# Performance work log

Measured on AMD Instinct MI355X. Metric: run time of the kernel, lower is better.

## Reference

```python
import jax, jax.numpy as jnp
import numpy as np

B, S, DIM = 2, 2048, 2048
H, DH = 16, 128            # head_dim = dim // n_heads; decop_rot_dim == head_dim (required by the view)
LKV, LQ = 512, 1024        # latent kv / q compression dims


def setup_inputs() -> dict:
    key = jax.random.key(0)
    ks = jax.random.split(key, 12)
    w = lambda k, shape: jax.random.normal(k, shape, jnp.float32) * 0.02
    x = jax.random.normal(ks[0], (B, S, DIM), jnp.float32)
    # rotary table: angles[t, i] = t * 10000^(-2i/DH), complex passed as cos/sin pair
    inv_freq = 1.0 / (10000.0 ** (np.arange(0, DH, 2, dtype=np.float64) / DH))
    ang = np.outer(np.arange(S, dtype=np.float64), inv_freq)  # [S, DH/2]
    return {
        "x": x,
        "freq_cos": jnp.asarray(np.cos(ang), jnp.float32),
        "freq_sin": jnp.asarray(np.sin(ang), jnp.float32),
        "w_lq": w(ks[1], (LQ, DIM)),
        "w_lkv": w(ks[2], (LKV, DIM)),
        "w_q": w(ks[3], (H * DH, LQ)),
        "w_k": w(ks[4], (H * DH, LKV)),
        "w_v": w(ks[5], (H * DH, LKV)),
        "w_qr": w(ks[6], (H * DH, LQ)),
        "b_qr": w(ks[7], (H * DH,)),
        "w_kr": w(ks[8], (H * DH, DIM)),
        "b_kr": w(ks[9], (H * DH,)),
        "w_o": w(ks[10], (DIM, H * DH)),
        "b_o": w(ks[11], (DIM,)),
    }


def _rope(t, freq):
    # t: [B,S,H,DH]; freq: [S,DH/2] complex. Pairs (even,odd) along last dim rotated.
    b, s, h, d = t.shape
    tc = t.astype(jnp.float32).reshape(b, s, h, d // 2, 2)
    tc = jax.lax.complex(tc[..., 0], tc[..., 1]) * freq[None, :, None, :]
    return jnp.stack([jnp.real(tc), jnp.imag(tc)], axis=-1).reshape(b, s, h, d).astype(t.dtype)


def reference(x, freq_cos, freq_sin, w_lq, w_lkv, w_q, w_k, w_v, w_qr, b_qr, w_kr, b_kr, w_o, b_o):
    b, s, _ = x.shape
    freq = jax.lax.complex(freq_cos, freq_sin)          # [S, DH/2]
    cq = x @ w_lq.T                                      # [B,S,LQ]
    ckv = x @ w_lkv.T                                    # [B,S,LKV]
    q = (cq @ w_q.T).reshape(b, s, H, DH)
    qr = _rope((cq @ w_qr.T + b_qr).reshape(b, s, H, DH), freq)
    k = (ckv @ w_k.T).reshape(b, s, H, DH)
    kr = _rope((x @ w_kr.T + b_kr).reshape(b, s, H, DH), freq)
    v = (ckv @ w_v.T).reshape(b, s, H, DH)
    q = jnp.concatenate([q, qr], axis=-1)                # [B,S,H,2*DH]
    k = jnp.concatenate([k, kr], axis=-1)
    # note: scale uses sqrt(head_dim), NOT sqrt(2*head_dim), faithful to source
    scores = jnp.einsum('bqhd,bkhd->bhqk', q, k) / jnp.sqrt(jnp.float32(DH))
    att = jax.nn.softmax(scores.astype(jnp.float32), axis=-1).astype(q.dtype)
    out = jnp.einsum('bhqk,bkhd->bqhd', att, v).reshape(b, s, H * DH)
    return out @ w_o.T + b_o
```

## Files before the change

### kernel.cpp

```cpp
#include <hip/hip_runtime.h>
#include <hip/hip_bf16.h>


#define Bb 2
#define Ss 2048
#define DIMd 2048
#define Hh 16
#define DHd 128

typedef __hip_bfloat16 bf16;
typedef __attribute__((ext_vector_type(8))) short short8;
typedef __attribute__((ext_vector_type(4))) float floatx4;
typedef __attribute__((ext_vector_type(16))) float floatx16;
typedef __attribute__((ext_vector_type(2))) unsigned int uintx2;

#define MFMA(a, b, c) __builtin_amdgcn_mfma_f32_16x16x32_bf16((a), (b), (c), 0, 0, 0)
#define MFMA32(a, b, c) __builtin_amdgcn_mfma_f32_32x32x16_bf16((a), (b), (c), 0, 0, 0)

__device__ __forceinline__ void async16(const bf16* g, bf16* l) {
  __builtin_amdgcn_global_load_lds(
      (const __attribute__((address_space(1))) unsigned int*)g,
      (__attribute__((address_space(3))) unsigned int*)l, 16, 0, 0);
}

__global__ __launch_bounds__(256) void cvt_all(
    const float* x, const float* wlq, const float* wlkv, const float* wq,
    const float* wqr, const float* wk, const float* wv, const float* wkr,
    const float* wo, bf16* dx, bf16* dwlq, bf16* dwlkv, bf16* dwq, bf16* dwqr,
    bf16* dwk, bf16* dwv, bf16* dwkr, bf16* dwo) {
  long i = (long)blockIdx.x * 256 + threadIdx.x;
  const float* src;
  bf16* dst;
  long base;
  if (i < 2097152L)      { src = x;    dst = dx;    base = 0; }
  else if (i < 2621440L) { src = wlq;  dst = dwlq;  base = 2097152L; }
  else if (i < 2883584L) { src = wlkv; dst = dwlkv; base = 2621440L; }
  else if (i < 3407872L) { src = wq;   dst = dwq;   base = 2883584L; }
  else if (i < 3932160L) { src = wqr;  dst = dwqr;  base = 3407872L; }
  else if (i < 4194304L) { src = wk;   dst = dwk;   base = 3932160L; }
  else if (i < 4456448L) { src = wv;   dst = dwv;   base = 4194304L; }
  else if (i < 5505024L) { src = wkr;  dst = dwkr;  base = 4456448L; }
  else                   { src = wo;   dst = dwo;   base = 5505024L; }
  long j = i - base;
  float4 f = ((const float4*)src)[j];
  union { ushort4 u4; bf16 h[4]; } cv;
  cv.h[0] = __float2bfloat16(f.x);
  cv.h[1] = __float2bfloat16(f.y);
  cv.h[2] = __float2bfloat16(f.z);
  cv.h[3] = __float2bfloat16(f.w);
  ((ushort4*)dst)[j] = cv.u4;
}

template <int MODE>
__device__ __forceinline__ void gemm_body(const bf16* __restrict__ A,
                                          const bf16* __restrict__ Bw,
                                          const float* __restrict__ bias,
                                          void* __restrict__ Cout,
                                          void* __restrict__ Cout2,
                                          const float* __restrict__ fco,
                                          const float* __restrict__ fsi,
                                          int M, int N, int K, int lda) {
  extern __shared__ __align__(16) bf16 smem[];
  bf16* As = smem;
  bf16* Bs = smem + 8192;
  const int tid = threadIdx.x;
  const int lane = tid & 63;
  const int w = tid >> 6;
  const int wm = w & 1, wn = w >> 1;
  const int m0 = blockIdx.y * 128, n0 = blockIdx.x * 128;
  const int lr = lane & 15, lg = lane >> 4;

  floatx4 acc[4][4];
#pragma unroll
  for (int mi = 0; mi < 4; ++mi)
#pragma unroll
    for (int ni = 0; ni < 4; ++ni)
#pragma unroll
      for (int r = 0; r < 4; ++r) acc[mi][ni][r] = 0.f;

  for (int k0 = 0; k0 < K; k0 += 64) {
    __syncthreads();
#pragma unroll
    for (int i = 0; i < 4; ++i) {
      int c = i * 256 + tid;
      int row = c >> 3;
      int cg = (c & 7) ^ (row & 7);
      async16(A + (size_t)(m0 + row) * lda + k0 + cg * 8, As + (i * 256 + w * 64) * 8);
      async16(Bw + (size_t)(n0 + row) * K + k0 + cg * 8, Bs + (i * 256 + w * 64) * 8);
    }
    __syncthreads();

#pragma unroll
    for (int ks = 0; ks < 2; ++ks) {
      short8 af[4], bfr[4];
#pragma unroll
      for (int mi = 0; mi < 4; ++mi) {
        int row = wm * 64 + mi * 16 + lr;
        af[mi] = *(const short8*)&As[row * 64 + (((ks * 4 + lg) ^ (lr & 7)) * 8)];
      }
#pragma unroll
      for (int ni = 0; ni < 4; ++ni) {
        int row = wn * 64 + ni * 16 + lr;
        bfr[ni] = *(const short8*)&Bs[row * 64 + (((ks * 4 + lg) ^ (lr & 7)) * 8)];
      }
#pragma unroll
      for (int mi = 0; mi < 4; ++mi)
#pragma unroll
        for (int ni = 0; ni < 4; ++ni)
          acc[mi][ni] = MFMA(af[mi], bfr[ni], acc[mi][ni]);
    }
  }

  if (MODE == 5 && n0 >= 2048) {
    __syncthreads();
#pragma unroll
    for (int mi = 0; mi < 4; ++mi)
#pragma unroll
      for (int ni = 0; ni < 4; ++ni)
#pragma unroll
        for (int r = 0; r < 4; ++r) {
          int ml = wm * 64 + mi * 16 + lg * 4 + r;
          int nl = wn * 64 + ni * 16 + lr;
          smem[ml * 129 + nl] = __float2bfloat16(acc[mi][ni][r]);
        }
    __syncthreads();
    int bb = m0 >> 11, s0 = m0 & 2047;
    int hh = (n0 - 2048) >> 7;
    short* vbase = (short*)Cout2 + ((size_t)(bb * Hh + hh) * 128) * Ss;
#pragma unroll
    for (int pa = 0; pa < 8; ++pa) {
      int d = pa * 16 + (tid >> 4);
      int sc = (tid & 15) * 8;
      short8 v;
#pragma unroll
      for (int i = 0; i < 8; ++i) v[i] = *(const short*)&smem[(sc + i) * 129 + d];
      *(short8*)(vbase + (size_t)d * Ss + s0 + sc) = v;
    }
    return;
  }

#pragma unroll
  for (int mi = 0; mi < 4; ++mi)
#pragma unroll
    for (int ni = 0; ni < 4; ++ni)
#pragma unroll
      for (int r = 0; r < 4; ++r) {
        int m = m0 + wm * 64 + mi * 16 + lg * 4 + r;
        int n = n0 + wn * 64 + ni * 16 + lr;
        float v = acc[mi][ni][r];
        int bb = m >> 11, s = m & 2047;
        if (MODE == 3) {
          v += bias[n];
          ((float*)Cout)[(size_t)m * N + n] = v;
        } else if (MODE == 4) {
          if (n < 2048) {
            int hh = n >> 7, d = n & 127;
            ((bf16*)Cout)[((size_t)((bb * Hh + hh) * Ss + s)) * 256 + d] =
                __float2bfloat16(v);
          } else {
            int n2 = n - 2048;
            int hh = n2 >> 7, d = n2 & 127;
            v += bias[n2];
            float vp = __shfl_xor(v, 1, 64);
            float co = fco[s * 64 + (d >> 1)];
            float sn = fsi[s * 64 + (d >> 1)];
            v = (d & 1) ? (v * co + vp * sn) : (v * co - vp * sn);
            ((bf16*)Cout)[((size_t)((bb * Hh + hh) * Ss + s)) * 256 + 128 + d] =
                __float2bfloat16(v);
          }
        } else if (MODE == 5) {
          int hh = n >> 7, d = n & 127;
          ((bf16*)Cout)[((size_t)((bb * Hh + hh) * Ss + s)) * 256 + d] =
              __float2bfloat16(v);
        } else if (MODE == 6) {
          if (n < 1536) {
            ((bf16*)Cout)[(size_t)m * 1536 + n] = __float2bfloat16(v);
          } else {
            int n2 = n - 1536;
            int hh = n2 >> 7, d = n2 & 127;
            v += bias[n2];
            float vp = __shfl_xor(v, 1, 64);
            float co = fco[s * 64 + (d >> 1)];
            float sn = fsi[s * 64 + (d >> 1)];
            v = (d & 1) ? (v * co + vp * sn) : (v * co - vp * sn);
            ((bf16*)Cout2)[((size_t)((bb * Hh + hh) * Ss + s)) * 256 + 128 + d] =
                __float2bfloat16(v);
          }
        }
      }
}

template <int MODE>
__global__ __launch_bounds__(256, 4) void gemm_bt(const bf16* __restrict__ A,
                                                  const bf16* __restrict__ Bw,
                                                  const float* __restrict__ bias,
                                                  void* __restrict__ Cout,
                                                  void* __restrict__ Cout2,
                                                  const float* __restrict__ fco,
                                                  const float* __restrict__ fsi,
                                                  int M, int N, int K, int lda) {
  gemm_body<MODE>(A, Bw, bias, Cout, Cout2, fco, fsi, M, N, K, lda);
}

__global__ __launch_bounds__(256, 4) void gemm_qkv(const bf16* __restrict__ ccat,
                                                   const bf16* __restrict__ wqcat,
                                                   const bf16* __restrict__ wkvcat,
                                                   const float* __restrict__ bqr,
                                                   void* __restrict__ qcat,
                                                   void* __restrict__ kcat,
                                                   void* __restrict__ vt,
                                                   const float* __restrict__ fco,
                                                   const float* __restrict__ fsi) {
  if (blockIdx.z == 0)
    gemm_body<4>(ccat, wqcat, bqr, qcat, nullptr, fco, fsi, 4096, 4096, 1024, 1536);
  else
    gemm_body<5>(ccat + 1024, wkvcat, nullptr, kcat, vt, nullptr, nullptr, 4096, 4096, 512, 1536);
}

#define FA_STAGE(KSN, VSN, J)                                                    \
  {                                                                              \
    _Pragma("unroll") for (int i = 0; i < 4; ++i) {                              \
      int r = w * 8 + i * 2 + (lane >> 5);                                       \
      async16(Kb + (size_t)((J) + r) * 256 + (((lane & 31) ^ (r & 7)) * 8),      \
              KSN + (w * 8 + i * 2) * 256);                                      \
    }                                                                            \
    _Pragma("unroll") for (int i = 0; i < 2; ++i) {                              \
      int d = w * 32 + i * 16 + (lane >> 2);                                     \
      async16(Vb + (size_t)d * Ss + (J) + (((lane & 3) ^ ((d >> 1) & 3)) * 8),   \
              VSN + (w * 32 + i * 16) * 32);                                     \
    }                                                                            \
  }

#define FA_COMPUTE(KP, VQ)                                                       \
  {                                                                              \
    floatx16 sf;                                                                 \
    _Pragma("unroll") for (int r = 0; r < 16; ++r) sf[r] = 0.f;                  \
    __builtin_amdgcn_s_setprio(1);                                               \
    _Pragma("unroll") for (int dt = 0; dt < 16; ++dt) {                          \
      short8 kf = *(const short8*)(KP[dt & 3] + (dt >> 2) * 64);                 \
      sf = MFMA32(kf, qf[dt], sf);                                               \
    }                                                                            \
    __builtin_amdgcn_s_setprio(0);                                               \
    unsigned pk[8];                                                              \
    _Pragma("unroll") for (int rp = 0; rp < 8; ++rp) {                           \
      float p0 = exp2f(sf[2 * rp] * CE);                                         \
      float p1 = exp2f(sf[2 * rp + 1] * CE);                                     \
      l += p0 + p1;                                                              \
      bf16 b0 = __float2bfloat16(p0);                                            \
      bf16 b1 = __float2bfloat16(p1);                                            \
      pk[rp] = ((unsigned)*(const unsigned short*)&b1 << 16) |                   \
               *(const unsigned short*)&b0;                                      \
    }                                                                            \
    __builtin_amdgcn_s_setprio(1);                                               \
    _Pragma("unroll") for (int kb = 0; kb < 2; ++kb) {                           \
      uintx2 w02 = __builtin_amdgcn_permlane32_swap(pk[kb * 4 + 0],              \
                                                    pk[kb * 4 + 2], false, false); \
      uintx2 w13 = __builtin_amdgcn_permlane32_swap(pk[kb * 4 + 1],              \
                                                    pk[kb * 4 + 3], false, false); \
      union { unsigned u[4]; short8 s; } pa;                                     \
      pa.u[0] = w02.x; pa.u[1] = w13.x; pa.u[2] = w02.y; pa.u[3] = w13.y;        \
      _Pragma("unroll") for (int nb = 0; nb < 4; ++nb) {                         \
        short8 vf = *(const short8*)(VQ[kb] + nb * 1024);                        \
        oacc[nb] = MFMA32(pa.s, vf, oacc[nb]);                                   \
      }                                                                          \
    }                                                                            \
    __builtin_amdgcn_s_setprio(0);                                               \
    __syncthreads();                                                             \
  }

__global__ __launch_bounds__(256, 2) void flash_attn(const bf16* __restrict__ Q,
                                                     const bf16* __restrict__ Kc,
                                                     const bf16* __restrict__ Vt,
                                                     bf16* __restrict__ Oa) {
  const float CE = 0.08838834764831845f * 1.4426950408889634f;
  __shared__ __align__(16) bf16 Ks0[32 * 256];
  __shared__ __align__(16) bf16 Ks1[32 * 256];
  __shared__ __align__(16) bf16 Vs0[128 * 32];
  __shared__ __align__(16) bf16 Vs1[128 * 32];

  const int lane = threadIdx.x & 63;
  const int w = threadIdx.x >> 6;
  const int m = lane & 31;
  const int hi = lane >> 5;
  const int bh = blockIdx.x;
  const int b = bh >> 4, h = bh & 15;
  const int q0 = blockIdx.y * 128 + w * 32;

  const bf16* Qb = Q + (size_t)bh * Ss * 256;
  const bf16* Kb = Kc + (size_t)bh * Ss * 256;
  const bf16* Vb = Vt + (size_t)bh * 128 * Ss;

  short8 qf[16];
  {
    const short* Qrow = (const short*)Qb + (size_t)(q0 + m) * 256 + hi * 8;
#pragma unroll
    for (int dt = 0; dt < 16; ++dt) qf[dt] = *(const short8*)(Qrow + dt * 16);
  }

  const int key = m & 7;
  const int vkey = (m >> 1) & 3;
  const short* kp0[4];
  const short* kp1[4];
#pragma unroll
  for (int dl = 0; dl < 4; ++dl) {
    int off = m * 256 + (((2 * dl + hi) ^ key) * 8);
    kp0[dl] = (const short*)Ks0 + off;
    kp1[dl] = (const short*)Ks1 + off;
  }
  const short* vq0[2];
  const short* vq1[2];
#pragma unroll
  for (int kb = 0; kb < 2; ++kb) {
    int off = m * 32 + (((2 * kb + hi) ^ vkey) * 8);
    vq0[kb] = (const short*)Vs0 + off;
    vq1[kb] = (const short*)Vs1 + off;
  }

  float l = 0.f;
  floatx16 oacc[4];
#pragma unroll
  for (int nb = 0; nb < 4; ++nb)
#pragma unroll
    for (int r = 0; r < 16; ++r) oacc[nb][r] = 0.f;

  FA_STAGE(Ks0, Vs0, 0);
  __syncthreads();

#pragma unroll 1
  for (int g = 0; g < 64; g += 2) {
    FA_STAGE(Ks1, Vs1, (g + 1) * 32);
    FA_COMPUTE(kp0, vq0);
    int jn = (g + 2) * 32;
    if (jn < Ss) FA_STAGE(Ks0, Vs0, jn);
    FA_COMPUTE(kp1, vq1);
  }

  float lsum = l + __shfl_xor(l, 32, 64);
  float inv = 1.f / lsum;

#pragma unroll
  for (int r = 0; r < 16; ++r) {
    int qr = (r & 3) + 8 * (r >> 2) + 4 * hi;
    float invr = __shfl(inv, (lane & 32) + qr, 64);
    int s = q0 + qr;
#pragma unroll
    for (int nb = 0; nb < 4; ++nb) {
      int d = nb * 32 + m;
      Oa[((size_t)(b * Ss + s)) * (Hh * 128) + h * 128 + d] =
          __float2bfloat16(oacc[nb][r] * invr);
    }
  }
}

extern "C" void kernel_launch(void* const* d_in, const int* in_sizes, int n_in,
                              void* d_out, int out_size, void* d_ws, size_t ws_size,
                              hipStream_t stream) {
  const float* x    = (const float*)d_in[0];
  const float* fco  = (const float*)d_in[1];
  const float* fsi  = (const float*)d_in[2];
  const float* wlq  = (const float*)d_in[3];
  const float* wlkv = (const float*)d_in[4];
  const float* wq   = (const float*)d_in[5];
  const float* wk   = (const float*)d_in[6];
  const float* wv   = (const float*)d_in[7];
  const float* wqr  = (const float*)d_in[8];
  const float* bqr  = (const float*)d_in[9];
  const float* wkr  = (const float*)d_in[10];
  const float* bkr  = (const float*)d_in[11];
  const float* wo   = (const float*)d_in[12];
  const float* bo   = (const float*)d_in[13];

  char* ws = (char*)d_ws;
  size_t o = 0;
  bf16* x_b    = (bf16*)(ws + o); o += (size_t)Bb * Ss * DIMd * 2;
  bf16* wbig   = (bf16*)(ws + o); o += (size_t)3584 * 2048 * 2;
  bf16* wqcat  = (bf16*)(ws + o); o += (size_t)4096 * 1024 * 2;
  bf16* wkvcat = (bf16*)(ws + o); o += (size_t)4096 * 512 * 2;
  bf16* wo_b   = (bf16*)(ws + o); o += (size_t)2048 * 2048 * 2;
  bf16* ccat   = (bf16*)(ws + o); o += (size_t)4096 * 1536 * 2;
  bf16* qcat   = (bf16*)(ws + o); o += (size_t)Bb * Hh * Ss * 256 * 2;
  bf16* kcat   = (bf16*)(ws + o); o += (size_t)Bb * Hh * Ss * 256 * 2;
  bf16* vt     = (bf16*)(ws + o); o += (size_t)Bb * Hh * 128 * Ss * 2;
  bf16* attn   = (bf16*)(ws + o); o += (size_t)4096 * 2048 * 2;

  cvt_all<<<25600, 256, 0, stream>>>(
      x, wlq, wlkv, wq, wqr, wk, wv, wkr, wo,
      x_b,
      wbig,
      wbig + (size_t)1024 * 2048,
      wqcat,
      wqcat + (size_t)2048 * 1024,
      wkvcat,
      wkvcat + (size_t)2048 * 512,
      wbig + (size_t)1536 * 2048,
      wo_b);

  const int M = Bb * Ss;
  const int GEMM_LDS = 128 * 129 * 2;
  gemm_bt<6><<<dim3(28, 32), 256, GEMM_LDS, stream>>>(
      x_b, wbig, bkr, ccat, kcat, fco, fsi, M, 3584, 2048, 2048);
  gemm_qkv<<<dim3(32, 32, 2), 256, GEMM_LDS, stream>>>(
      ccat, wqcat, wkvcat, bqr, qcat, kcat, vt, fco, fsi);

  flash_attn<<<dim3(Bb * Hh, Ss / 128), 256, 0, stream>>>(qcat, kcat, vt, attn);

  gemm_bt<3><<<dim3(16, 32), 256, GEMM_LDS, stream>>>(
      attn, wo_b, bo, (float*)d_out, nullptr, nullptr, nullptr, M, 2048, 2048, 2048);
}
```

Baseline: 457.4 us.

## Add 256x256-tile 4-stage pipelined GEMM for projection and Q GEMMs

Introduces a new gemm8 kernel with 512 threads, 256x256 output tiles, K-step 32 and a 4-deep async global-to-LDS ring buffer using 128KB dynamic shared memory, with MFMA priority hints. It replaces the first projection GEMM and the Q part of the fused QKV GEMM, while the KV part now runs as a separate gemm_bt launch. The larger tiles are meant to raise arithmetic intensity and hide load latency. In exchange, occupancy drops and the grids become small (224 and 256 blocks), which may underfill the CUs. Splitting one launch into two also adds serialization.

```diff
diff --git a/kernel.cpp b/kernel.cpp
--- a/kernel.cpp
+++ b/kernel.cpp
@@ -202,19 +202,132 @@
   gemm_body<MODE>(A, Bw, bias, Cout, Cout2, fco, fsi, M, N, K, lda);
 }
 
-__global__ __launch_bounds__(256, 4) void gemm_qkv(const bf16* __restrict__ ccat,
-                                                   const bf16* __restrict__ wqcat,
-                                                   const bf16* __restrict__ wkvcat,
-                                                   const float* __restrict__ bqr,
-                                                   void* __restrict__ qcat,
-                                                   void* __restrict__ kcat,
-                                                   void* __restrict__ vt,
-                                                   const float* __restrict__ fco,
-                                                   const float* __restrict__ fsi) {
-  if (blockIdx.z == 0)
-    gemm_body<4>(ccat, wqcat, bqr, qcat, nullptr, fco, fsi, 4096, 4096, 1024, 1536);
-  else
-    gemm_body<5>(ccat + 1024, wkvcat, nullptr, kcat, vt, nullptr, nullptr, 4096, 4096, 512, 1536);
+#define G8_STAGE(TT)                                                           \
+  {                                                                            \
+    bf16* db = smem + ((TT) & 3) * 16384;                                      \
+    const int kk0 = (TT) * 32;                                                 \
+    _Pragma("unroll") for (int i = 0; i < 2; ++i) {                            \
+      int c = i * 512 + tid;                                                   \
+      int row = c >> 2;                                                        \
+      int cg = (c & 3) ^ ((row >> 1) & 3);                                     \
+      async16(A + (size_t)(m0 + row) * lda + kk0 + cg * 8, db + c * 8);        \
+    }                                                                          \
+    _Pragma("unroll") for (int i = 0; i < 2; ++i) {                            \
+      int c = i * 512 + tid;                                                   \
+      int row = c >> 2;                                                        \
+      int cg = (c & 3) ^ ((row >> 1) & 3);                                     \
+      async16(Bw + (size_t)(n0 + row) * KTOT + kk0 + cg * 8,                   \
+              db + 8192 + c * 8);                                              \
+    }                                                                          \
+  }
+
+#define G8_COMPUTE(TT)                                                         \
+  {                                                                            \
+    const bf16* cb = smem + ((TT) & 3) * 16384;                                \
+    short8 bfr[4];                                                             \
+    _Pragma("unroll") for (int ni = 0; ni < 4; ++ni) {                         \
+      int row = wn * 64 + ni * 16 + lr;                                        \
+      bfr[ni] = *(const short8*)&cb[8192 + row * 32 +                          \
+                                    ((lg ^ ((row >> 1) & 3)) * 8)];            \
+    }                                                                          \
+    short8 af[8];                                                              \
+    _Pragma("unroll") for (int mi = 0; mi < 8; ++mi) {                         \
+      int row = wm * 128 + mi * 16 + lr;                                       \
+      af[mi] = *(const short8*)&cb[row * 32 + ((lg ^ ((row >> 1) & 3)) * 8)];  \
+    }                                                                          \
+    __builtin_amdgcn_s_setprio(1);                                             \
+    _Pragma("unroll") for (int mi = 0; mi < 8; ++mi)                           \
+      _Pragma("unroll") for (int ni = 0; ni < 4; ++ni)                         \
+          acc[mi][ni] = MFMA(af[mi], bfr[ni], acc[mi][ni]);                    \
+    __builtin_amdgcn_s_setprio(0);                                             \
+  }
+
+template <int MODE, int KTOT>
+__global__ __launch_bounds__(512, 2) void gemm8(const bf16* __restrict__ A,
+                                                const bf16* __restrict__ Bw,
+                                                const float* __restrict__ bias,
+                                                void* __restrict__ Cout,
+                                                void* __restrict__ Cout2,
+                                                const float* __restrict__ fco,
+                                                const float* __restrict__ fsi,
+                                                int M, int N, int lda) {
+  extern __shared__ __align__(16) bf16 smem[];
+  constexpr int NT = KTOT / 32;
+  const int tid = threadIdx.x;
+  const int lane = tid & 63;
+  const int w = tid >> 6;
+  const int wm = w >> 2, wn = w & 3;
+  const int m0 = blockIdx.y * 256, n0 = blockIdx.x * 256;
+  const int lr = lane & 15, lg = lane >> 4;
+
+  floatx4 acc[8][4];
+#pragma unroll
+  for (int mi = 0; mi < 8; ++mi)
+#pragma unroll
+    for (int ni = 0; ni < 4; ++ni)
+#pragma unroll
+      for (int r = 0; r < 4; ++r) acc[mi][ni][r] = 0.f;
+
+  G8_STAGE(0);
+  G8_STAGE(1);
+  G8_STAGE(2);
+
+#pragma unroll 1
+  for (int t = 0; t < NT - 2; ++t) {
+    asm volatile("s_waitcnt vmcnt(8)" ::: "memory");
+    __builtin_amdgcn_s_barrier();
+    if (t < NT - 3) G8_STAGE(t + 3);
+    G8_COMPUTE(t);
+  }
+  asm volatile("s_waitcnt vmcnt(4)" ::: "memory");
+  __builtin_amdgcn_s_barrier();
+  G8_COMPUTE(NT - 2);
+  asm volatile("s_waitcnt vmcnt(0)" ::: "memory");
+  __builtin_amdgcn_s_barrier();
+  G8_COMPUTE(NT - 1);
+
+#pragma unroll
+  for (int mi = 0; mi < 8; ++mi)
+#pragma unroll
+    for (int ni = 0; ni < 4; ++ni)
+#pragma unroll
+      for (int r = 0; r < 4; ++r) {
+        int m = m0 + wm * 128 + mi * 16 + lg * 4 + r;
+        int n = n0 + wn * 64 + ni * 16 + lr;
+        float v = acc[mi][ni][r];
+        int bb = m >> 11, s = m & 2047;
+        if (MODE == 4) {
+          if (n < 2048) {
+            int hh = n >> 7, d = n & 127;
+            ((bf16*)Cout)[((size_t)((bb * Hh + hh) * Ss + s)) * 256 + d] =
+                __float2bfloat16(v);
+          } else {
+            int n2 = n - 2048;
+            int hh = n2 >> 7, d = n2 & 127;
+            v += bias[n2];
+            float vp = __shfl_xor(v, 1, 64);
+            float co = fco[s * 64 + (d >> 1)];
+            float sn = fsi[s * 64 + (d >> 1)];
+            v = (d & 1) ? (v * co + vp * sn) : (v * co - vp * sn);
+            ((bf16*)Cout)[((size_t)((bb * Hh + hh) * Ss + s)) * 256 + 128 + d] =
+                __float2bfloat16(v);
+          }
+        } else if (MODE == 6) {
+          if (n < 1536) {
+            ((bf16*)Cout)[(size_t)m * 1536 + n] = __float2bfloat16(v);
+          } else {
+            int n2 = n - 1536;
+            int hh = n2 >> 7, d = n2 & 127;
+            v += bias[n2];
+            float vp = __shfl_xor(v, 1, 64);
+            float co = fco[s * 64 + (d >> 1)];
+            float sn = fsi[s * 64 + (d >> 1)];
+            v = (d & 1) ? (v * co + vp * sn) : (v * co - vp * sn);
+            ((bf16*)Cout2)[((size_t)((bb * Hh + hh) * Ss + s)) * 256 + 128 + d] =
+                __float2bfloat16(v);
+          }
+        }
+      }
 }
 
 #define FA_STAGE(KSN, VSN, J)                                                    \
@@ -383,6 +496,15 @@
   bf16* vt     = (bf16*)(ws + o); o += (size_t)Bb * Hh * 128 * Ss * 2;
   bf16* attn   = (bf16*)(ws + o); o += (size_t)4096 * 2048 * 2;
 
+  static bool g8init = false;
+  if (!g8init) {
+    hipFuncSetAttribute(reinterpret_cast<const void*>(gemm8<6, 2048>),
+                        hipFuncAttributeMaxDynamicSharedMemorySize, 131072);
+    hipFuncSetAttribute(reinterpret_cast<const void*>(gemm8<4, 1024>),
+                        hipFuncAttributeMaxDynamicSharedMemorySize, 131072);
+    g8init = true;
+  }
+
   cvt_all<<<25600, 256, 0, stream>>>(
       x, wlq, wlkv, wq, wqr, wk, wv, wkr, wo,
       x_b,
@@ -397,10 +519,13 @@
 
   const int M = Bb * Ss;
   const int GEMM_LDS = 128 * 129 * 2;
-  gemm_bt<6><<<dim3(28, 32), 256, GEMM_LDS, stream>>>(
-      x_b, wbig, bkr, ccat, kcat, fco, fsi, M, 3584, 2048, 2048);
-  gemm_qkv<<<dim3(32, 32, 2), 256, GEMM_LDS, stream>>>(
-      ccat, wqcat, wkvcat, bqr, qcat, kcat, vt, fco, fsi);
+
+  gemm8<6, 2048><<<dim3(14, 16), 512, 131072, stream>>>(
+      x_b, wbig, bkr, ccat, kcat, fco, fsi, M, 3584, 2048);
+  gemm8<4, 1024><<<dim3(16, 16), 512, 131072, stream>>>(
+      ccat, wqcat, bqr, qcat, nullptr, fco, fsi, M, 4096, 1536);
+  gemm_bt<5><<<dim3(32, 32), 256, GEMM_LDS, stream>>>(
+      ccat + 1024, wkvcat, nullptr, kcat, vt, nullptr, nullptr, M, 4096, 512, 1536);
 
   flash_attn<<<dim3(Bb * Hh, Ss / 128), 256, 0, stream>>>(qcat, kcat, vt, attn);
 
```

After: 496.9 us. +8.6%, slower.

## Triple-buffer flash attention and software-pipeline QK^T with PV across tiles

Applied to the files above, without the earlier changes.

The flash attention loop moves from double to triple LDS buffers. It is restructured so the PV product of tile t-1 and the QK^T plus exp of tile t run between split barriers. A partial vmcnt wait replaces the full __syncthreads, so async global-to-LDS loads can stay in flight longer. The softmax scale times log2(e) is now folded into the Q projection epilogue, which removes a multiply per score. This raises LDS use per block and makes the prologue and epilogue more intricate.

```diff
diff --git a/kernel.cpp b/kernel.cpp
--- a/kernel.cpp
+++ b/kernel.cpp
@@ -16,6 +16,8 @@
 
 #define MFMA(a, b, c) __builtin_amdgcn_mfma_f32_16x16x32_bf16((a), (b), (c), 0, 0, 0)
 #define MFMA32(a, b, c) __builtin_amdgcn_mfma_f32_32x32x16_bf16((a), (b), (c), 0, 0, 0)
+
+#define CEF (0.08838834764831845f * 1.4426950408889634f)
 
 __device__ __forceinline__ void async16(const bf16* g, bf16* l) {
   __builtin_amdgcn_global_load_lds(
@@ -156,7 +158,7 @@
           if (n < 2048) {
             int hh = n >> 7, d = n & 127;
             ((bf16*)Cout)[((size_t)((bb * Hh + hh) * Ss + s)) * 256 + d] =
-                __float2bfloat16(v);
+                __float2bfloat16(v * CEF);
           } else {
             int n2 = n - 2048;
             int hh = n2 >> 7, d = n2 & 127;
@@ -166,7 +168,7 @@
             float sn = fsi[s * 64 + (d >> 1)];
             v = (d & 1) ? (v * co + vp * sn) : (v * co - vp * sn);
             ((bf16*)Cout)[((size_t)((bb * Hh + hh) * Ss + s)) * 256 + 128 + d] =
-                __float2bfloat16(v);
+                __float2bfloat16(v * CEF);
           }
         } else if (MODE == 5) {
           int hh = n >> 7, d = n & 127;
@@ -231,9 +233,8 @@
     }                                                                            \
   }
 
-#define FA_COMPUTE(KP, VQ)                                                       \
+#define FA_QKT(KP)                                                               \
   {                                                                              \
-    floatx16 sf;                                                                 \
     _Pragma("unroll") for (int r = 0; r < 16; ++r) sf[r] = 0.f;                  \
     __builtin_amdgcn_s_setprio(1);                                               \
     _Pragma("unroll") for (int dt = 0; dt < 16; ++dt) {                          \
@@ -241,16 +242,23 @@
       sf = MFMA32(kf, qf[dt], sf);                                               \
     }                                                                            \
     __builtin_amdgcn_s_setprio(0);                                               \
-    unsigned pk[8];                                                              \
+  }
+
+#define FA_SM()                                                                  \
+  {                                                                              \
     _Pragma("unroll") for (int rp = 0; rp < 8; ++rp) {                           \
-      float p0 = exp2f(sf[2 * rp] * CE);                                         \
-      float p1 = exp2f(sf[2 * rp + 1] * CE);                                     \
+      float p0 = exp2f(sf[2 * rp]);                                              \
+      float p1 = exp2f(sf[2 * rp + 1]);                                          \
       l += p0 + p1;                                                              \
       bf16 b0 = __float2bfloat16(p0);                                            \
       bf16 b1 = __float2bfloat16(p1);                                            \
       pk[rp] = ((unsigned)*(const unsigned short*)&b1 << 16) |                   \
                *(const unsigned short*)&b0;                                      \
     }                                                                            \
+  }
+
+#define FA_PV(VQ)                                                                \
+  {                                                                              \
     __builtin_amdgcn_s_setprio(1);                                               \
     _Pragma("unroll") for (int kb = 0; kb < 2; ++kb) {                           \
       uintx2 w02 = __builtin_amdgcn_permlane32_swap(pk[kb * 4 + 0],              \
@@ -265,18 +273,26 @@
       }                                                                          \
     }                                                                            \
     __builtin_amdgcn_s_setprio(0);                                               \
-    __syncthreads();                                                             \
-  }
+  }
+
+#define FA_BODY(VQpv, KPqk, KSst, VSst, Jst)                                     \
+  FA_STAGE(KSst, VSst, Jst);                                                     \
+  FA_PV(VQpv);                                                                   \
+  asm volatile("s_waitcnt vmcnt(6)" ::: "memory");                               \
+  __builtin_amdgcn_s_barrier();                                                  \
+  FA_QKT(KPqk);                                                                  \
+  FA_SM();
 
 __global__ __launch_bounds__(256, 2) void flash_attn(const bf16* __restrict__ Q,
                                                      const bf16* __restrict__ Kc,
                                                      const bf16* __restrict__ Vt,
                                                      bf16* __restrict__ Oa) {
-  const float CE = 0.08838834764831845f * 1.4426950408889634f;
   __shared__ __align__(16) bf16 Ks0[32 * 256];
   __shared__ __align__(16) bf16 Ks1[32 * 256];
+  __shared__ __align__(16) bf16 Ks2[32 * 256];
   __shared__ __align__(16) bf16 Vs0[128 * 32];
   __shared__ __align__(16) bf16 Vs1[128 * 32];
+  __shared__ __align__(16) bf16 Vs2[128 * 32];
 
   const int lane = threadIdx.x & 63;
   const int w = threadIdx.x >> 6;
@@ -299,24 +315,26 @@
 
   const int key = m & 7;
   const int vkey = (m >> 1) & 3;
-  const short* kp0[4];
-  const short* kp1[4];
+  const short *kp0[4], *kp1[4], *kp2[4];
 #pragma unroll
   for (int dl = 0; dl < 4; ++dl) {
     int off = m * 256 + (((2 * dl + hi) ^ key) * 8);
     kp0[dl] = (const short*)Ks0 + off;
     kp1[dl] = (const short*)Ks1 + off;
-  }
-  const short* vq0[2];
-  const short* vq1[2];
+    kp2[dl] = (const short*)Ks2 + off;
+  }
+  const short *vq0[2], *vq1[2], *vq2[2];
 #pragma unroll
   for (int kb = 0; kb < 2; ++kb) {
     int off = m * 32 + (((2 * kb + hi) ^ vkey) * 8);
     vq0[kb] = (const short*)Vs0 + off;
     vq1[kb] = (const short*)Vs1 + off;
+    vq2[kb] = (const short*)Vs2 + off;
   }
 
   float l = 0.f;
+  floatx16 sf;
+  unsigned pk[8];
   floatx16 oacc[4];
 #pragma unroll
   for (int nb = 0; nb < 4; ++nb)
@@ -324,16 +342,27 @@
     for (int r = 0; r < 16; ++r) oacc[nb][r] = 0.f;
 
   FA_STAGE(Ks0, Vs0, 0);
-  __syncthreads();
+  FA_STAGE(Ks1, Vs1, 32);
+  asm volatile("s_waitcnt vmcnt(6)" ::: "memory");
+  __builtin_amdgcn_s_barrier();
+  FA_QKT(kp0);
+  FA_SM();
 
 #pragma unroll 1
-  for (int g = 0; g < 64; g += 2) {
-    FA_STAGE(Ks1, Vs1, (g + 1) * 32);
-    FA_COMPUTE(kp0, vq0);
-    int jn = (g + 2) * 32;
-    if (jn < Ss) FA_STAGE(Ks0, Vs0, jn);
-    FA_COMPUTE(kp1, vq1);
-  }
+  for (int c = 0; c < 20; ++c) {
+    const int j2 = (3 * c + 2) * 32;
+    FA_BODY(vq0, kp1, Ks2, Vs2, j2);
+    FA_BODY(vq1, kp2, Ks0, Vs0, j2 + 32);
+    FA_BODY(vq2, kp0, Ks1, Vs1, j2 + 64);
+  }
+  FA_BODY(vq0, kp1, Ks2, Vs2, 62 * 32);
+  FA_BODY(vq1, kp2, Ks0, Vs0, 63 * 32);
+  FA_PV(vq2);
+  asm volatile("s_waitcnt vmcnt(0)" ::: "memory");
+  __builtin_amdgcn_s_barrier();
+  FA_QKT(kp0);
+  FA_SM();
+  FA_PV(vq0);
 
   float lsum = l + __shfl_xor(l, 32, 64);
   float inv = 1.f / lsum;
```

Result: no change. 454.5 us (median of 2 runs) (-0.6%).

## Load V directly from global in MFMA layout, fold softmax scale into Q

Applied to the files above, without the earlier changes.

The V-projection epilogue now writes V in a blocked layout, with 8-key groups each holding every head-dim column, so each lane can fetch its MFMA B-operand fragments straight from global memory into registers. This drops the V shared-memory staging buffers and their async copies. The softmax scale times log2(e) is folded into Q when Q is written, which removes a multiply per score. The QK^T accumulation is also split into two independent MFMA chains to shorten the dependency chain. In exchange, every wave issues uncached-style global loads for V on each tile, which raises register pressure and adds global latency that is no longer shared through LDS.

```diff
diff --git a/kernel.cpp b/kernel.cpp
--- a/kernel.cpp
+++ b/kernel.cpp
@@ -16,6 +16,8 @@
 
 #define MFMA(a, b, c) __builtin_amdgcn_mfma_f32_16x16x32_bf16((a), (b), (c), 0, 0, 0)
 #define MFMA32(a, b, c) __builtin_amdgcn_mfma_f32_32x32x16_bf16((a), (b), (c), 0, 0, 0)
+
+#define CEF (0.08838834764831845f * 1.4426950408889634f)
 
 __device__ __forceinline__ void async16(const bf16* g, bf16* l) {
   __builtin_amdgcn_global_load_lds(
@@ -134,7 +136,7 @@
       short8 v;
 #pragma unroll
       for (int i = 0; i < 8; ++i) v[i] = *(const short*)&smem[(sc + i) * 129 + d];
-      *(short8*)(vbase + (size_t)d * Ss + s0 + sc) = v;
+      *(short8*)(vbase + ((size_t)((s0 + sc) >> 3)) * 1024 + d * 8) = v;
     }
     return;
   }
@@ -156,7 +158,7 @@
           if (n < 2048) {
             int hh = n >> 7, d = n & 127;
             ((bf16*)Cout)[((size_t)((bb * Hh + hh) * Ss + s)) * 256 + d] =
-                __float2bfloat16(v);
+                __float2bfloat16(v * CEF);
           } else {
             int n2 = n - 2048;
             int hh = n2 >> 7, d = n2 & 127;
@@ -166,7 +168,7 @@
             float sn = fsi[s * 64 + (d >> 1)];
             v = (d & 1) ? (v * co + vp * sn) : (v * co - vp * sn);
             ((bf16*)Cout)[((size_t)((bb * Hh + hh) * Ss + s)) * 256 + 128 + d] =
-                __float2bfloat16(v);
+                __float2bfloat16(v * CEF);
           }
         } else if (MODE == 5) {
           int hh = n >> 7, d = n & 127;
@@ -217,34 +219,37 @@
     gemm_body<5>(ccat + 1024, wkvcat, nullptr, kcat, vt, nullptr, nullptr, 4096, 4096, 512, 1536);
 }
 
-#define FA_STAGE(KSN, VSN, J)                                                    \
+#define FA_STAGE_K(KSN, J)                                                       \
   {                                                                              \
     _Pragma("unroll") for (int i = 0; i < 4; ++i) {                              \
       int r = w * 8 + i * 2 + (lane >> 5);                                       \
       async16(Kb + (size_t)((J) + r) * 256 + (((lane & 31) ^ (r & 7)) * 8),      \
               KSN + (w * 8 + i * 2) * 256);                                      \
     }                                                                            \
-    _Pragma("unroll") for (int i = 0; i < 2; ++i) {                              \
-      int d = w * 32 + i * 16 + (lane >> 2);                                     \
-      async16(Vb + (size_t)d * Ss + (J) + (((lane & 3) ^ ((d >> 1) & 3)) * 8),   \
-              VSN + (w * 32 + i * 16) * 32);                                     \
-    }                                                                            \
-  }
-
-#define FA_COMPUTE(KP, VQ)                                                       \
+  }
+
+#define FA_BODY(KP, KSN, Jv, Jst, DO_STAGE)                                      \
   {                                                                              \
-    floatx16 sf;                                                                 \
-    _Pragma("unroll") for (int r = 0; r < 16; ++r) sf[r] = 0.f;                  \
+    short8 vr[8];                                                                \
+    _Pragma("unroll") for (int kb = 0; kb < 2; ++kb)                             \
+      _Pragma("unroll") for (int nb = 0; nb < 4; ++nb)                           \
+        vr[kb * 4 + nb] = *(const short8*)(                                      \
+            Vb2 + (size_t)(((Jv) >> 3) + 2 * kb + hi) * 1024 + (nb * 32 + m) * 8); \
+    if (DO_STAGE) FA_STAGE_K(KSN, Jst);                                          \
+    floatx16 se, so;                                                             \
+    _Pragma("unroll") for (int r = 0; r < 16; ++r) { se[r] = 0.f; so[r] = 0.f; } \
     __builtin_amdgcn_s_setprio(1);                                               \
     _Pragma("unroll") for (int dt = 0; dt < 16; ++dt) {                          \
       short8 kf = *(const short8*)(KP[dt & 3] + (dt >> 2) * 64);                 \
-      sf = MFMA32(kf, qf[dt], sf);                                               \
+      if (dt & 1) so = MFMA32(kf, qf[dt], so);                                   \
+      else        se = MFMA32(kf, qf[dt], se);                                   \
     }                                                                            \
     __builtin_amdgcn_s_setprio(0);                                               \
+    floatx16 sf = se + so;                                                       \
     unsigned pk[8];                                                              \
     _Pragma("unroll") for (int rp = 0; rp < 8; ++rp) {                           \
-      float p0 = exp2f(sf[2 * rp] * CE);                                         \
-      float p1 = exp2f(sf[2 * rp + 1] * CE);                                     \
+      float p0 = exp2f(sf[2 * rp]);                                              \
+      float p1 = exp2f(sf[2 * rp + 1]);                                          \
       l += p0 + p1;                                                              \
       bf16 b0 = __float2bfloat16(p0);                                            \
       bf16 b1 = __float2bfloat16(p1);                                            \
@@ -259,10 +264,8 @@
                                                     pk[kb * 4 + 3], false, false); \
       union { unsigned u[4]; short8 s; } pa;                                     \
       pa.u[0] = w02.x; pa.u[1] = w13.x; pa.u[2] = w02.y; pa.u[3] = w13.y;        \
-      _Pragma("unroll") for (int nb = 0; nb < 4; ++nb) {                         \
-        short8 vf = *(const short8*)(VQ[kb] + nb * 1024);                        \
-        oacc[nb] = MFMA32(pa.s, vf, oacc[nb]);                                   \
-      }                                                                          \
+      _Pragma("unroll") for (int nb = 0; nb < 4; ++nb)                           \
+        oacc[nb] = MFMA32(pa.s, vr[kb * 4 + nb], oacc[nb]);                      \
     }                                                                            \
     __builtin_amdgcn_s_setprio(0);                                               \
     __syncthreads();                                                             \
@@ -272,11 +275,8 @@
                                                      const bf16* __restrict__ Kc,
                                                      const bf16* __restrict__ Vt,
                                                      bf16* __restrict__ Oa) {
-  const float CE = 0.08838834764831845f * 1.4426950408889634f;
   __shared__ __align__(16) bf16 Ks0[32 * 256];
   __shared__ __align__(16) bf16 Ks1[32 * 256];
-  __shared__ __align__(16) bf16 Vs0[128 * 32];
-  __shared__ __align__(16) bf16 Vs1[128 * 32];
 
   const int lane = threadIdx.x & 63;
   const int w = threadIdx.x >> 6;
@@ -288,7 +288,7 @@
 
   const bf16* Qb = Q + (size_t)bh * Ss * 256;
   const bf16* Kb = Kc + (size_t)bh * Ss * 256;
-  const bf16* Vb = Vt + (size_t)bh * 128 * Ss;
+  const short* Vb2 = (const short*)Vt + (size_t)bh * 128 * Ss;
 
   short8 qf[16];
   {
@@ -298,23 +298,13 @@
   }
 
   const int key = m & 7;
-  const int vkey = (m >> 1) & 3;
-  const short* kp0[4];
-  const short* kp1[4];
+  const short *kp0[4], *kp1[4];
 #pragma unroll
   for (int dl = 0; dl < 4; ++dl) {
     int off = m * 256 + (((2 * dl + hi) ^ key) * 8);
     kp0[dl] = (const short*)Ks0 + off;
     kp1[dl] = (const short*)Ks1 + off;
   }
-  const short* vq0[2];
-  const short* vq1[2];
-#pragma unroll
-  for (int kb = 0; kb < 2; ++kb) {
-    int off = m * 32 + (((2 * kb + hi) ^ vkey) * 8);
-    vq0[kb] = (const short*)Vs0 + off;
-    vq1[kb] = (const short*)Vs1 + off;
-  }
 
   float l = 0.f;
   floatx16 oacc[4];
@@ -323,16 +313,14 @@
 #pragma unroll
     for (int r = 0; r < 16; ++r) oacc[nb][r] = 0.f;
 
-  FA_STAGE(Ks0, Vs0, 0);
+  FA_STAGE_K(Ks0, 0);
   __syncthreads();
 
 #pragma unroll 1
-  for (int g = 0; g < 64; g += 2) {
-    FA_STAGE(Ks1, Vs1, (g + 1) * 32);
-    FA_COMPUTE(kp0, vq0);
-    int jn = (g + 2) * 32;
-    if (jn < Ss) FA_STAGE(Ks0, Vs0, jn);
-    FA_COMPUTE(kp1, vq1);
+  for (int it = 0; it < 32; ++it) {
+    const int j = it * 64;
+    FA_BODY(kp0, Ks1, j, j + 32, true);
+    FA_BODY(kp1, Ks0, j + 32, j + 64, (j + 64) < Ss);
   }
 
   float lsum = l + __shfl_xor(l, 32, 64);
```

New measurement: 483.0 us. 1.06x slower.
